# Performance work log

Hardware: AMD Instinct MI355X
Metric: run time of the kernel (lower is better)

The kernel has to match this reference:

```python
import jax, jax.numpy as jnp
import numpy as np
jax.config.update("jax_enable_x64", True)

SR = 44100
STATE_SIZE = 4096
RG0, R10, C10, C20 = 1.0e6, 4.7e5, 3.3e-9, 1.0e-9

# Reconstructed DK-method incidence matrices (3 circuit nodes, 1 vsrc):
#   Vin at node1; C1 node1->node2; R1 node2->gnd; pot top node2->node3;
#   pot bottom node3->gnd; C2 node3->gnd; output at node3 (pot wiper).
_Nu = np.array([[1., 0., 0.]])
_Nx = np.array([[1., -1., 0.], [0., 0., 1.]])
_Nr = np.array([[0., 1., 0.]])
_Nv = np.array([[0., 1., -1.], [0., 0., 1.]])
_No = np.array([[0., 0., 1.]])


def _preamp_forward(x, cond, state, alpha_rg, alpha_r1, alpha_c1, alpha_c2, cond_w, cond_b):
    f64 = jnp.float64
    T = 1.0 / SR
    Nu, Nx, Nr, Nv, No = (jnp.asarray(m, f64) for m in (_Nu, _Nx, _Nr, _Nv, _No))
    Zm = jnp.eye(2, dtype=f64)
    n_nodes, n_vsrc = 3, 1
    zpad = jnp.zeros((2, n_vsrc), f64)
    Nvp = jnp.concatenate([Nv, zpad], axis=1)                      # [2,4]
    Nxp = jnp.concatenate([Nx, zpad], axis=1)                      # [2,4]
    Nop = jnp.concatenate([No, jnp.zeros((1, n_vsrc), f64)], 1)    # [1,4]
    Nup = jnp.concatenate([jnp.zeros((n_nodes, n_vsrc), f64), jnp.eye(n_vsrc, dtype=f64)], 0)  # [4,1]

    # component updates (sigmoid-trimmed around nominal values)
    RG = (0.9 + jax.nn.sigmoid(alpha_rg[0]).astype(f64) * 0.2) * RG0
    R1 = (0.99 + jax.nn.sigmoid(alpha_r1[0]).astype(f64) * 0.02) * R10
    C1 = (0.9 + jax.nn.sigmoid(alpha_c1[0]).astype(f64) * 0.2) * C10
    C2 = (0.9 + jax.nn.sigmoid(alpha_c2[0]).astype(f64) * 0.2) * C20
    Gr = jnp.reshape(1.0 / R1, (1, 1))
    Gx = jnp.diag(jnp.stack([2.0 * C1 / T, 2.0 * C2 / T]))

    # cond block: affine -> sigmoid -> log pot taper
    pot = jax.nn.sigmoid(cond[:, 0] * cond_w[0] + cond_b[0])
    p = jnp.clip((jnp.power(10.0, pot) - 1.0) / 9.0, 1e-4, 1.0 - 1e-4).astype(f64)  # [B]

    # state-space update
    top = jnp.concatenate([Nr.T @ Gr @ Nr + Nx.T @ Gx @ Nx, Nu.T], axis=1)
    bot = jnp.concatenate([Nu, jnp.zeros((n_vsrc, n_vsrc), f64)], axis=1)
    So_inv = jnp.linalg.inv(jnp.concatenate([top, bot], axis=0))   # [4,4]
    Q = Nvp @ So_inv @ Nvp.T                                        # [2,2]
    Ux = Nxp @ So_inv @ Nvp.T                                       # [2,2]
    Uo = Nop @ So_inv @ Nvp.T                                       # [1,2]
    Uu = Nup.T @ So_inv @ Nvp.T                                     # [1,2]
    ZGx = 2.0 * Zm @ Gx
    Ao = ZGx @ Nxp @ So_inv @ Nxp.T - Zm
    Bo = ZGx @ Nxp @ So_inv @ Nup
    Do = Nop @ So_inv @ Nxp.T
    Eo = Nop @ So_inv @ Nup

    d = jnp.stack([(1.0 - p) * RG, p * RG], axis=-1)                # [B,2]
    Rv = d[:, :, None] * jnp.eye(2, dtype=f64)                      # [B,2,2] diag
    RvQ = jnp.linalg.inv(Rv + Q)                                    # [B,2,2]

    ZGxUx = ZGx @ Ux
    A = Ao - ZGxUx @ RvQ @ Ux.T                                     # [B,2,2]
    Bm = Bo - ZGxUx @ RvQ @ Uu.T                                    # [B,2,1]
    Dm = Do - Uo @ RvQ @ Ux.T                                       # [B,1,2]
    Em = Eo - Uo @ RvQ @ Uu.T                                       # [B,1,1]

    # quadratic characteristic poly [1, -tr, det] (= real part of prod(z-eig))
    def poly2(M):
        tr = M[..., 0, 0] + M[..., 1, 1]
        det = M[..., 0, 0] * M[..., 1, 1] - M[..., 0, 1] * M[..., 1, 0]
        return jnp.stack([jnp.ones_like(tr), -tr, det], axis=-1)    # [B,3]

    den = poly2(A)
    num = poly2(A - Bm @ Dm) + (Em[:, 0] - 1.0) * den

    nb = 1 + STATE_SIZE // 2
    z = jnp.exp(-1j * jnp.linspace(0.0, jnp.pi, nb))                # complex128 [nb]

    def polyval(c):  # Horner, highest degree first
        c = c.astype(jnp.complex128)
        return (c[:, 0, None] * z + c[:, 1, None]) * z + c[:, 2, None]  # [B,nb]

    h = polyval(num) / polyval(den)                                 # [B,nb]

    L = x.shape[1]
    st = jnp.concatenate([state[:, L:, :], x], axis=1).astype(f64)  # [B,S,1]
    sf = jnp.fft.rfft(st, axis=1)                                   # [B,nb,1]
    out = jnp.fft.irfft(sf * h[:, :, None], axis=1).astype(jnp.float32)
    return out[:, -L:, :]


def setup_inputs() -> dict:
    key = jax.random.key(0)
    k0, k1, k2 = jax.random.split(key, 3)
    B, L = 2048, 2048
    return {
        "x": jax.random.normal(k0, (B, L, 1), dtype=jnp.float32),
        "cond": jax.random.uniform(k1, (B, 1), dtype=jnp.float32),
        "state": jax.random.normal(k2, (B, STATE_SIZE, 1), dtype=jnp.float32) * 0.1,
        "alpha_rg": jnp.zeros((1,), jnp.float32),
        "alpha_r1": jnp.zeros((1,), jnp.float32),
        "alpha_c1": jnp.zeros((1,), jnp.float32),
        "alpha_c2": jnp.zeros((1,), jnp.float32),
        "cond_w": jnp.ones((1,), jnp.float32),
        "cond_b": jnp.zeros((1,), jnp.float32),
    }


def reference(x, cond, state, alpha_rg, alpha_r1, alpha_c1, alpha_c2, cond_w, cond_b):
    return _preamp_forward(x, cond, state, alpha_rg, alpha_r1, alpha_c1, alpha_c2, cond_w, cond_b)
```

## Files before the change

### kernel.cpp

```cpp
#include <hip/hip_runtime.h>
#include <math.h>

#define NFFT 4096
#define HALF 2048
#define LSEG 2048
#define SSZ 4096

static __device__ __forceinline__ double sigm_f32(float v) {
    return (double)(1.0f / (1.0f + expf(-v)));
}

static __device__ void inv4(const double a[4][4], double out[4][4]) {
    double m[4][8];
    for (int i = 0; i < 4; ++i) {
        for (int j = 0; j < 4; ++j) { m[i][j] = a[i][j]; m[i][j + 4] = (i == j) ? 1.0 : 0.0; }
    }
    for (int c = 0; c < 4; ++c) {
        int piv = c; double best = fabs(m[c][c]);
        for (int r = c + 1; r < 4; ++r) { double v = fabs(m[r][c]); if (v > best) { best = v; piv = r; } }
        if (piv != c) for (int j = 0; j < 8; ++j) { double t = m[c][j]; m[c][j] = m[piv][j]; m[piv][j] = t; }
        double d = 1.0 / m[c][c];
        for (int j = 0; j < 8; ++j) m[c][j] *= d;
        for (int r = 0; r < 4; ++r) {
            if (r == c) continue;
            double f = m[r][c];
            for (int j = 0; j < 8; ++j) m[r][j] -= f * m[c][j];
        }
    }
    for (int i = 0; i < 4; ++i) for (int j = 0; j < 4; ++j) out[i][j] = m[i][j + 4];
}

__global__ void preamp_coef_kernel(const float* __restrict__ cond,
                                   const float* __restrict__ a_rg,
                                   const float* __restrict__ a_r1,
                                   const float* __restrict__ a_c1,
                                   const float* __restrict__ a_c2,
                                   const float* __restrict__ cond_w,
                                   const float* __restrict__ cond_b,
                                   double* __restrict__ coef, int B) {
    int b = blockIdx.x * blockDim.x + threadIdx.x;
    if (b >= B) return;

    const double T = 1.0 / 44100.0;
    const double RG = (0.9 + sigm_f32(a_rg[0]) * 0.2) * 1.0e6;
    const double R1 = (0.99 + sigm_f32(a_r1[0]) * 0.02) * 4.7e5;
    const double C1 = (0.9 + sigm_f32(a_c1[0]) * 0.2) * 3.3e-9;
    const double C2 = (0.9 + sigm_f32(a_c2[0]) * 0.2) * 1.0e-9;
    const double g1 = 1.0 / R1;
    const double gc1 = 2.0 * C1 / T;
    const double gc2 = 2.0 * C2 / T;

    float zf = cond[b] * cond_w[0] + cond_b[0];
    float pot = 1.0f / (1.0f + expf(-zf));
    float pr = (powf(10.0f, pot) - 1.0f) / 9.0f;
    pr = fminf(fmaxf(pr, 1e-4f), 1.0f - 1e-4f);
    double p = (double)pr;

    double So[4][4] = {
        { gc1,     -gc1,      0.0, 1.0},
        {-gc1,      gc1 + g1, 0.0, 0.0},
        { 0.0,      0.0,      gc2, 0.0},
        { 1.0,      0.0,      0.0, 0.0}};
    double S[4][4];
    inv4(So, S);

    double Q00 = S[1][1] - S[1][2] - S[2][1] + S[2][2];
    double Q01 = S[1][2] - S[2][2];
    double Q10 = S[2][1] - S[2][2];
    double Q11 = S[2][2];

    double Ux00 = S[0][1] - S[0][2] - S[1][1] + S[1][2];
    double Ux01 = S[0][2] - S[1][2];
    double Ux10 = S[2][1] - S[2][2];
    double Ux11 = S[2][2];

    double Uo0 = S[2][1] - S[2][2], Uo1 = S[2][2];
    double Uu0 = S[3][1] - S[3][2], Uu1 = S[3][2];

    double P00 = S[0][0] - S[0][1] - S[1][0] + S[1][1];
    double P01 = S[0][2] - S[1][2];
    double P10 = S[2][0] - S[2][1];
    double P11 = S[2][2];

    double Ao00 = 2.0 * gc1 * P00 - 1.0, Ao01 = 2.0 * gc1 * P01;
    double Ao10 = 2.0 * gc2 * P10,       Ao11 = 2.0 * gc2 * P11 - 1.0;

    double Bo0 = 2.0 * gc1 * (S[0][3] - S[1][3]);
    double Bo1 = 2.0 * gc2 * S[2][3];

    double Do0 = S[2][0] - S[2][1], Do1 = S[2][2];
    double Eo  = S[2][3];

    double T00 = 2.0 * gc1 * Ux00, T01 = 2.0 * gc1 * Ux01;
    double T10 = 2.0 * gc2 * Ux10, T11 = 2.0 * gc2 * Ux11;

    double d0 = (1.0 - p) * RG, d1v = p * RG;
    double M00 = d0 + Q00, M01 = Q01, M10 = Q10, M11 = d1v + Q11;
    double idet = 1.0 / (M00 * M11 - M01 * M10);
    double G00 =  M11 * idet, G01 = -M01 * idet;
    double G10 = -M10 * idet, G11 =  M00 * idet;

    double TG00 = T00 * G00 + T01 * G10, TG01 = T00 * G01 + T01 * G11;
    double TG10 = T10 * G00 + T11 * G10, TG11 = T10 * G01 + T11 * G11;

    double A00 = Ao00 - (TG00 * Ux00 + TG01 * Ux01);
    double A01 = Ao01 - (TG00 * Ux10 + TG01 * Ux11);
    double A10 = Ao10 - (TG10 * Ux00 + TG11 * Ux01);
    double A11 = Ao11 - (TG10 * Ux10 + TG11 * Ux11);

    double Bm0 = Bo0 - (TG00 * Uu0 + TG01 * Uu1);
    double Bm1 = Bo1 - (TG10 * Uu0 + TG11 * Uu1);

    double w0v = Uo0 * G00 + Uo1 * G10, w1v = Uo0 * G01 + Uo1 * G11;
    double Dm0 = Do0 - (w0v * Ux00 + w1v * Ux01);
    double Dm1 = Do1 - (w0v * Ux10 + w1v * Ux11);
    double Em  = Eo  - (w0v * Uu0 + w1v * Uu1);

    double den1 = -(A00 + A11);
    double den2 = A00 * A11 - A01 * A10;
    double Mm00 = A00 - Bm0 * Dm0, Mm01 = A01 - Bm0 * Dm1;
    double Mm10 = A10 - Bm1 * Dm0, Mm11 = A11 - Bm1 * Dm1;
    double num0 = Em;
    double num1 = -(Mm00 + Mm11) + (Em - 1.0) * den1;
    double num2 = (Mm00 * Mm11 - Mm01 * Mm10) + (Em - 1.0) * den2;

    coef[(size_t)b * 5 + 0] = num0;
    coef[(size_t)b * 5 + 1] = num1;
    coef[(size_t)b * 5 + 2] = num2;
    coef[(size_t)b * 5 + 3] = den1;
    coef[(size_t)b * 5 + 4] = den2;
}


static __device__ __forceinline__ float2 cmul(float2 a, float2 b) {
    return make_float2(a.x * b.x - a.y * b.y, a.x * b.y + a.y * b.x);
}
static __device__ __forceinline__ float2 cadd(float2 a, float2 b) { return make_float2(a.x + b.x, a.y + b.y); }
static __device__ __forceinline__ float2 csub(float2 a, float2 b) { return make_float2(a.x - b.x, a.y - b.y); }

static __device__ __forceinline__ int PAD(int i) { return i + (i >> 4); }

template <int SGN>
static __device__ __forceinline__ void dft16(float2 r[16]) {
    const float S = (float)SGN;
    float2 t[16];
#pragma unroll
    for (int n1 = 0; n1 < 4; ++n1) {
        float2 a = r[n1], b = r[n1 + 4], c = r[n1 + 8], d = r[n1 + 12];
        float2 A = cadd(a, c), B = cadd(b, d), C = csub(a, c), D = csub(b, d);
        float2 iD = make_float2(-S * D.y, S * D.x);
        t[n1 * 4 + 0] = cadd(A, B);
        t[n1 * 4 + 1] = cadd(C, iD);
        t[n1 * 4 + 2] = csub(A, B);
        t[n1 * 4 + 3] = csub(C, iD);
    }
    const float CC[10] = {1.f, 0.92387953251f, 0.70710678119f, 0.38268343236f, 0.f,
                          -0.38268343236f, -0.70710678119f, -0.92387953251f, -1.f, -0.92387953251f};
    const float SS[10] = {0.f, 0.38268343236f, 0.70710678119f, 0.92387953251f, 1.f,
                          0.92387953251f, 0.70710678119f, 0.38268343236f, 0.f, -0.38268343236f};
#pragma unroll
    for (int n1 = 1; n1 < 4; ++n1) {
#pragma unroll
        for (int m2 = 1; m2 < 4; ++m2) {
            const int k = n1 * m2;
            t[n1 * 4 + m2] = cmul(t[n1 * 4 + m2], make_float2(CC[k], S * SS[k]));
        }
    }
#pragma unroll
    for (int m2 = 0; m2 < 4; ++m2) {
        float2 a = t[m2], b = t[4 + m2], c = t[8 + m2], d = t[12 + m2];
        float2 A = cadd(a, c), B = cadd(b, d), C = csub(a, c), D = csub(b, d);
        float2 iD = make_float2(-S * D.y, S * D.x);
        r[m2]      = cadd(A, B);
        r[m2 + 4]  = cadd(C, iD);
        r[m2 + 8]  = csub(A, B);
        r[m2 + 12] = csub(C, iD);
    }
}

static __device__ __forceinline__ void twiddle_chain(float2 r[16], float2 w1) {
    float2 w2 = cmul(w1, w1);
    float2 w3 = cmul(w2, w1);
    float2 w4 = cmul(w2, w2);
    float2 w5 = cmul(w4, w1);
    float2 w6 = cmul(w4, w2);
    float2 w7 = cmul(w4, w3);
    float2 w8 = cmul(w4, w4);
    r[1] = cmul(r[1], w1);   r[2] = cmul(r[2], w2);
    r[3] = cmul(r[3], w3);   r[4] = cmul(r[4], w4);
    r[5] = cmul(r[5], w5);   r[6] = cmul(r[6], w6);
    r[7] = cmul(r[7], w7);   r[8] = cmul(r[8], w8);
    r[9]  = cmul(r[9],  cmul(w8, w1));
    r[10] = cmul(r[10], cmul(w8, w2));
    r[11] = cmul(r[11], cmul(w8, w3));
    r[12] = cmul(r[12], cmul(w8, w4));
    r[13] = cmul(r[13], cmul(w8, w5));
    r[14] = cmul(r[14], cmul(w8, w6));
    r[15] = cmul(r[15], cmul(w8, w7));
}

static __device__ __forceinline__ float2 eval_h(double n0, double n1, double n2,
                                                double d1, double d2,
                                                double zr, double zi) {
    double ar = n0 * zr + n1, ai = n0 * zi;
    double nr = ar * zr - ai * zi + n2, ni = ar * zi + ai * zr;
    double br = zr + d1, bi = zi;
    double dr = br * zr - bi * zi + d2, di = br * zi + bi * zr;
    float fnr = (float)nr, fni = (float)ni, fdr = (float)dr, fdi = (float)di;
    float idn = __builtin_amdgcn_rcpf(fdr * fdr + fdi * fdi);
    return make_float2((fnr * fdr + fni * fdi) * idn,
                       (fni * fdr - fnr * fdi) * idn);
}

__global__ __launch_bounds__(256)
void preamp_fft_kernel(const float* __restrict__ x,
                       const float* __restrict__ state,
                       const double* __restrict__ coef,
                       float* __restrict__ out, int B) {
    __shared__ float2 a_s[NFFT + NFFT / 16];

    const int t = threadIdx.x;
    const int b0 = 2 * blockIdx.x;
    const int b1 = (b0 + 1 < B) ? b0 + 1 : b0;

    const float* st0 = state + (size_t)b0 * SSZ + (SSZ - LSEG);
    const float* xb0 = x + (size_t)b0 * LSEG;
    const float* st1 = state + (size_t)b1 * SSZ + (SSZ - LSEG);
    const float* xb1 = x + (size_t)b1 * LSEG;

    for (int i = t; i < NFFT; i += 256) {
        float fa, fb;
        if (i < LSEG) { fa = st0[i]; fb = st1[i]; }
        else          { fa = xb0[i - LSEG]; fb = xb1[i - LSEG]; }
        a_s[PAD(i)] = make_float2(fa, fb);
    }
    __syncthreads();

    const float TW4096 = 0.00153398078788564f;
    const float TW256  = 0.02454369260617026f;

    float2 r[16];

#pragma unroll
    for (int m = 0; m < 16; ++m) r[m] = a_s[PAD(t + 256 * m)];
    dft16<-1>(r);
    {
        float sw, cw;
        __sincosf((float)t * TW4096, &sw, &cw);
        twiddle_chain(r, make_float2(cw, -sw));
    }
#pragma unroll
    for (int m = 0; m < 16; ++m) a_s[PAD(t + 256 * m)] = r[m];
    __syncthreads();

    {
        const int sub = t >> 4, j = t & 15;
        const int base = sub * 256 + j;
#pragma unroll
        for (int m = 0; m < 16; ++m) r[m] = a_s[PAD(base + 16 * m)];
        dft16<-1>(r);
        float sw, cw;
        __sincosf((float)j * TW256, &sw, &cw);
        twiddle_chain(r, make_float2(cw, -sw));
#pragma unroll
        for (int m = 0; m < 16; ++m) a_s[PAD(base + 16 * m)] = r[m];
    }
    __syncthreads();

    {
        const int base = 16 * t;
#pragma unroll
        for (int m = 0; m < 16; ++m) r[m] = a_s[PAD(base + m)];
        dft16<-1>(r);
        const int klo = ((t & 15) << 4) | (t >> 4);
        __syncthreads();
#pragma unroll
        for (int m = 0; m < 16; ++m) a_s[PAD((m << 8) | klo)] = r[m];
    }
    __syncthreads();

    {
        const double na0 = coef[(size_t)b0 * 5 + 0];
        const double na1 = coef[(size_t)b0 * 5 + 1];
        const double na2 = coef[(size_t)b0 * 5 + 2];
        const double da1 = coef[(size_t)b0 * 5 + 3];
        const double da2 = coef[(size_t)b0 * 5 + 4];
        const double nb0 = coef[(size_t)b1 * 5 + 0];
        const double nb1 = coef[(size_t)b1 * 5 + 1];
        const double nb2 = coef[(size_t)b1 * 5 + 2];
        const double db1 = coef[(size_t)b1 * 5 + 3];
        const double db2 = coef[(size_t)b1 * 5 + 4];

        for (int i = t; i <= HALF; i += 256) {
            const int k  = i;
            const int kr = (NFFT - i) & (NFFT - 1);
            float2 Wk = a_s[PAD(k)];
            float2 Wr = a_s[PAD(kr)];
            float Xar = 0.5f * (Wk.x + Wr.x), Xai = 0.5f * (Wk.y - Wr.y);
            float Xbr = 0.5f * (Wk.y + Wr.y), Xbi = 0.5f * (Wr.x - Wk.x);
            float sw, cw;
            __sincosf((float)k * TW4096, &sw, &cw);
            const double zr = (double)cw, zi = -(double)sw;
            float2 Ha = eval_h(na0, na1, na2, da1, da2, zr, zi);
            float2 Hb = eval_h(nb0, nb1, nb2, db1, db2, zr, zi);
            float Yar = Ha.x * Xar - Ha.y * Xai, Yai = Ha.x * Xai + Ha.y * Xar;
            float Ybr = Hb.x * Xbr - Hb.y * Xbi, Ybi = Hb.x * Xbi + Hb.y * Xbr;
            a_s[PAD(k)] = make_float2(Yar - Ybi, Yai + Ybr);
            if (kr != k) a_s[PAD(kr)] = make_float2(Yar + Ybi, Ybr - Yai);
        }
    }
    __syncthreads();

    {
        const int base = 16 * t;
        const int klo = ((t & 15) << 4) | (t >> 4);
#pragma unroll
        for (int m = 0; m < 16; ++m) r[m] = a_s[PAD((m << 8) | klo)];
        dft16<1>(r);
        __syncthreads();
#pragma unroll
        for (int m = 0; m < 16; ++m) a_s[PAD(base + m)] = r[m];
    }
    __syncthreads();

    {
        const int sub = t >> 4, j = t & 15;
        const int base = sub * 256 + j;
#pragma unroll
        for (int m = 0; m < 16; ++m) r[m] = a_s[PAD(base + 16 * m)];
        float sw, cw;
        __sincosf((float)j * TW256, &sw, &cw);
        twiddle_chain(r, make_float2(cw, sw));
        dft16<1>(r);
#pragma unroll
        for (int m = 0; m < 16; ++m) a_s[PAD(base + 16 * m)] = r[m];
    }
    __syncthreads();

    {
#pragma unroll
        for (int m = 0; m < 16; ++m) r[m] = a_s[PAD(t + 256 * m)];
        float sw, cw;
        __sincosf((float)t * TW4096, &sw, &cw);
        twiddle_chain(r, make_float2(cw, sw));
        dft16<1>(r);
        const float scale = 1.0f / (float)NFFT;
        float* ob0 = out + (size_t)b0 * LSEG;
        float* ob1 = out + (size_t)b1 * LSEG;
#pragma unroll
        for (int m = 8; m < 16; ++m) {
            ob0[t + 256 * (m - 8)] = r[m].x * scale;
            if (b1 != b0) ob1[t + 256 * (m - 8)] = r[m].y * scale;
        }
    }
}

extern "C" void kernel_launch(void* const* d_in, const int* in_sizes, int n_in,
                              void* d_out, int out_size, void* d_ws, size_t ws_size,
                              hipStream_t stream) {
    const float* x     = (const float*)d_in[0];
    const float* cond  = (const float*)d_in[1];
    const float* state = (const float*)d_in[2];
    const float* a_rg  = (const float*)d_in[3];
    const float* a_r1  = (const float*)d_in[4];
    const float* a_c1  = (const float*)d_in[5];
    const float* a_c2  = (const float*)d_in[6];
    const float* c_w   = (const float*)d_in[7];
    const float* c_b   = (const float*)d_in[8];
    float* out = (float*)d_out;

    const int B = in_sizes[1];
    double* coef = (double*)d_ws;

    preamp_coef_kernel<<<dim3((B + 255) / 256), dim3(256), 0, stream>>>(
        cond, a_rg, a_r1, a_c1, a_c2, c_w, c_b, coef, B);
    preamp_fft_kernel<<<dim3((B + 1) / 2), dim3(256), 0, stream>>>(x, state, coef, out, B);
}
```

Baseline: 126.2 us.

## Fuse coefficient computation into FFT kernel and evaluate transfer function in fp32

Removes the separate coefficient kernel: two threads per block compute the per-batch filter coefficients (using a closed-form inverse of the 4x4 system instead of Gauss-Jordan) and publish them through shared memory. The frequency-response evaluation is rewritten around u = z-1 using a half-angle sine/cosine and fully float arithmetic, replacing the double-precision polynomial evaluation. This cuts a kernel launch, the global coefficient round-trip and the fp64 work in the spectral multiply, at the risk of reduced accuracy in the filter response near DC.

```diff
diff --git a/kernel.cpp b/kernel.cpp
--- a/kernel.cpp
+++ b/kernel.cpp
@@ -5,131 +5,6 @@
 #define HALF 2048
 #define LSEG 2048
 #define SSZ 4096
-
-static __device__ __forceinline__ double sigm_f32(float v) {
-    return (double)(1.0f / (1.0f + expf(-v)));
-}
-
-static __device__ void inv4(const double a[4][4], double out[4][4]) {
-    double m[4][8];
-    for (int i = 0; i < 4; ++i) {
-        for (int j = 0; j < 4; ++j) { m[i][j] = a[i][j]; m[i][j + 4] = (i == j) ? 1.0 : 0.0; }
-    }
-    for (int c = 0; c < 4; ++c) {
-        int piv = c; double best = fabs(m[c][c]);
-        for (int r = c + 1; r < 4; ++r) { double v = fabs(m[r][c]); if (v > best) { best = v; piv = r; } }
-        if (piv != c) for (int j = 0; j < 8; ++j) { double t = m[c][j]; m[c][j] = m[piv][j]; m[piv][j] = t; }
-        double d = 1.0 / m[c][c];
-        for (int j = 0; j < 8; ++j) m[c][j] *= d;
-        for (int r = 0; r < 4; ++r) {
-            if (r == c) continue;
-            double f = m[r][c];
-            for (int j = 0; j < 8; ++j) m[r][j] -= f * m[c][j];
-        }
-    }
-    for (int i = 0; i < 4; ++i) for (int j = 0; j < 4; ++j) out[i][j] = m[i][j + 4];
-}
-
-__global__ void preamp_coef_kernel(const float* __restrict__ cond,
-                                   const float* __restrict__ a_rg,
-                                   const float* __restrict__ a_r1,
-                                   const float* __restrict__ a_c1,
-                                   const float* __restrict__ a_c2,
-                                   const float* __restrict__ cond_w,
-                                   const float* __restrict__ cond_b,
-                                   double* __restrict__ coef, int B) {
-    int b = blockIdx.x * blockDim.x + threadIdx.x;
-    if (b >= B) return;
-
-    const double T = 1.0 / 44100.0;
-    const double RG = (0.9 + sigm_f32(a_rg[0]) * 0.2) * 1.0e6;
-    const double R1 = (0.99 + sigm_f32(a_r1[0]) * 0.02) * 4.7e5;
-    const double C1 = (0.9 + sigm_f32(a_c1[0]) * 0.2) * 3.3e-9;
-    const double C2 = (0.9 + sigm_f32(a_c2[0]) * 0.2) * 1.0e-9;
-    const double g1 = 1.0 / R1;
-    const double gc1 = 2.0 * C1 / T;
-    const double gc2 = 2.0 * C2 / T;
-
-    float zf = cond[b] * cond_w[0] + cond_b[0];
-    float pot = 1.0f / (1.0f + expf(-zf));
-    float pr = (powf(10.0f, pot) - 1.0f) / 9.0f;
-    pr = fminf(fmaxf(pr, 1e-4f), 1.0f - 1e-4f);
-    double p = (double)pr;
-
-    double So[4][4] = {
-        { gc1,     -gc1,      0.0, 1.0},
-        {-gc1,      gc1 + g1, 0.0, 0.0},
-        { 0.0,      0.0,      gc2, 0.0},
-        { 1.0,      0.0,      0.0, 0.0}};
-    double S[4][4];
-    inv4(So, S);
-
-    double Q00 = S[1][1] - S[1][2] - S[2][1] + S[2][2];
-    double Q01 = S[1][2] - S[2][2];
-    double Q10 = S[2][1] - S[2][2];
-    double Q11 = S[2][2];
-
-    double Ux00 = S[0][1] - S[0][2] - S[1][1] + S[1][2];
-    double Ux01 = S[0][2] - S[1][2];
-    double Ux10 = S[2][1] - S[2][2];
-    double Ux11 = S[2][2];
-
-    double Uo0 = S[2][1] - S[2][2], Uo1 = S[2][2];
-    double Uu0 = S[3][1] - S[3][2], Uu1 = S[3][2];
-
-    double P00 = S[0][0] - S[0][1] - S[1][0] + S[1][1];
-    double P01 = S[0][2] - S[1][2];
-    double P10 = S[2][0] - S[2][1];
-    double P11 = S[2][2];
-
-    double Ao00 = 2.0 * gc1 * P00 - 1.0, Ao01 = 2.0 * gc1 * P01;
-    double Ao10 = 2.0 * gc2 * P10,       Ao11 = 2.0 * gc2 * P11 - 1.0;
-
-    double Bo0 = 2.0 * gc1 * (S[0][3] - S[1][3]);
-    double Bo1 = 2.0 * gc2 * S[2][3];
-
-    double Do0 = S[2][0] - S[2][1], Do1 = S[2][2];
-    double Eo  = S[2][3];
-
-    double T00 = 2.0 * gc1 * Ux00, T01 = 2.0 * gc1 * Ux01;
-    double T10 = 2.0 * gc2 * Ux10, T11 = 2.0 * gc2 * Ux11;
-
-    double d0 = (1.0 - p) * RG, d1v = p * RG;
-    double M00 = d0 + Q00, M01 = Q01, M10 = Q10, M11 = d1v + Q11;
-    double idet = 1.0 / (M00 * M11 - M01 * M10);
-    double G00 =  M11 * idet, G01 = -M01 * idet;
-    double G10 = -M10 * idet, G11 =  M00 * idet;
-
-    double TG00 = T00 * G00 + T01 * G10, TG01 = T00 * G01 + T01 * G11;
-    double TG10 = T10 * G00 + T11 * G10, TG11 = T10 * G01 + T11 * G11;
-
-    double A00 = Ao00 - (TG00 * Ux00 + TG01 * Ux01);
-    double A01 = Ao01 - (TG00 * Ux10 + TG01 * Ux11);
-    double A10 = Ao10 - (TG10 * Ux00 + TG11 * Ux01);
-    double A11 = Ao11 - (TG10 * Ux10 + TG11 * Ux11);
-
-    double Bm0 = Bo0 - (TG00 * Uu0 + TG01 * Uu1);
-    double Bm1 = Bo1 - (TG10 * Uu0 + TG11 * Uu1);
-
-    double w0v = Uo0 * G00 + Uo1 * G10, w1v = Uo0 * G01 + Uo1 * G11;
-    double Dm0 = Do0 - (w0v * Ux00 + w1v * Ux01);
-    double Dm1 = Do1 - (w0v * Ux10 + w1v * Ux11);
-    double Em  = Eo  - (w0v * Uu0 + w1v * Uu1);
-
-    double den1 = -(A00 + A11);
-    double den2 = A00 * A11 - A01 * A10;
-    double Mm00 = A00 - Bm0 * Dm0, Mm01 = A01 - Bm0 * Dm1;
-    double Mm10 = A10 - Bm1 * Dm0, Mm11 = A11 - Bm1 * Dm1;
-    double num0 = Em;
-    double num1 = -(Mm00 + Mm11) + (Em - 1.0) * den1;
-    double num2 = (Mm00 * Mm11 - Mm01 * Mm10) + (Em - 1.0) * den2;
-
-    coef[(size_t)b * 5 + 0] = num0;
-    coef[(size_t)b * 5 + 1] = num1;
-    coef[(size_t)b * 5 + 2] = num2;
-    coef[(size_t)b * 5 + 3] = den1;
-    coef[(size_t)b * 5 + 4] = den2;
-}
 
 
 static __device__ __forceinline__ float2 cmul(float2 a, float2 b) {
@@ -199,25 +74,19 @@
     r[15] = cmul(r[15], cmul(w8, w7));
 }
 
-static __device__ __forceinline__ float2 eval_h(double n0, double n1, double n2,
-                                                double d1, double d2,
-                                                double zr, double zi) {
-    double ar = n0 * zr + n1, ai = n0 * zi;
-    double nr = ar * zr - ai * zi + n2, ni = ar * zi + ai * zr;
-    double br = zr + d1, bi = zi;
-    double dr = br * zr - bi * zi + d2, di = br * zi + bi * zr;
-    float fnr = (float)nr, fni = (float)ni, fdr = (float)dr, fdi = (float)di;
-    float idn = __builtin_amdgcn_rcpf(fdr * fdr + fdi * fdi);
-    return make_float2((fnr * fdr + fni * fdi) * idn,
-                       (fni * fdr - fnr * fdi) * idn);
-}
-
 __global__ __launch_bounds__(256)
 void preamp_fft_kernel(const float* __restrict__ x,
                        const float* __restrict__ state,
-                       const double* __restrict__ coef,
+                       const float* __restrict__ cond,
+                       const float* __restrict__ a_rg,
+                       const float* __restrict__ a_r1,
+                       const float* __restrict__ a_c1,
+                       const float* __restrict__ a_c2,
+                       const float* __restrict__ cond_w,
+                       const float* __restrict__ cond_b,
                        float* __restrict__ out, int B) {
     __shared__ float2 a_s[NFFT + NFFT / 16];
+    __shared__ float cf[10];
 
     const int t = threadIdx.x;
     const int b0 = 2 * blockIdx.x;
@@ -234,10 +103,104 @@
         else          { fa = xb0[i - LSEG]; fb = xb1[i - LSEG]; }
         a_s[PAD(i)] = make_float2(fa, fb);
     }
+
+    if ((t & 127) == 0) {
+        const int who = t >> 7;
+        const int bb = who ? b1 : b0;
+
+        const double T = 1.0 / 44100.0;
+        const double RG = (0.9 + (double)(1.0f / (1.0f + expf(-a_rg[0]))) * 0.2) * 1.0e6;
+        const double R1 = (0.99 + (double)(1.0f / (1.0f + expf(-a_r1[0]))) * 0.02) * 4.7e5;
+        const double C1 = (0.9 + (double)(1.0f / (1.0f + expf(-a_c1[0]))) * 0.2) * 3.3e-9;
+        const double C2 = (0.9 + (double)(1.0f / (1.0f + expf(-a_c2[0]))) * 0.2) * 1.0e-9;
+        const double g1 = 1.0 / R1;
+        const double gc1 = 2.0 * C1 * 44100.0;  (void)T;
+        const double gc2 = 2.0 * C2 * 44100.0;
+
+        float zf = cond[bb] * cond_w[0] + cond_b[0];
+        float pot = 1.0f / (1.0f + expf(-zf));
+        float prf = (powf(10.0f, pot) - 1.0f) / 9.0f;
+        prf = fminf(fmaxf(prf, 1e-4f), 1.0f - 1e-4f);
+        const double p = (double)prf;
+
+        const double ds = gc1 + g1;
+        double S[4][4] = {
+            {0.0, 0.0,        0.0,       1.0},
+            {0.0, 1.0 / ds,   0.0,       gc1 / ds},
+            {0.0, 0.0,        1.0 / gc2, 0.0},
+            {1.0, gc1 / ds,   0.0,       -gc1 * g1 / ds}};
+
+        double Q00 = S[1][1] - S[1][2] - S[2][1] + S[2][2];
+        double Q01 = S[1][2] - S[2][2];
+        double Q10 = S[2][1] - S[2][2];
+        double Q11 = S[2][2];
+
+        double Ux00 = S[0][1] - S[0][2] - S[1][1] + S[1][2];
+        double Ux01 = S[0][2] - S[1][2];
+        double Ux10 = S[2][1] - S[2][2];
+        double Ux11 = S[2][2];
+
+        double Uo0 = S[2][1] - S[2][2], Uo1 = S[2][2];
+        double Uu0 = S[3][1] - S[3][2], Uu1 = S[3][2];
+
+        double P00 = S[0][0] - S[0][1] - S[1][0] + S[1][1];
+        double P01 = S[0][2] - S[1][2];
+        double P10 = S[2][0] - S[2][1];
+        double P11 = S[2][2];
+
+        double Ao00 = 2.0 * gc1 * P00 - 1.0, Ao01 = 2.0 * gc1 * P01;
+        double Ao10 = 2.0 * gc2 * P10,       Ao11 = 2.0 * gc2 * P11 - 1.0;
+
+        double Bo0 = 2.0 * gc1 * (S[0][3] - S[1][3]);
+        double Bo1 = 2.0 * gc2 * S[2][3];
+
+        double Do0 = S[2][0] - S[2][1], Do1 = S[2][2];
+        double Eo  = S[2][3];
+
+        double T00 = 2.0 * gc1 * Ux00, T01 = 2.0 * gc1 * Ux01;
+        double T10 = 2.0 * gc2 * Ux10, T11 = 2.0 * gc2 * Ux11;
+
+        double d0 = (1.0 - p) * RG, d1v = p * RG;
+        double M00 = d0 + Q00, M01 = Q01, M10 = Q10, M11 = d1v + Q11;
+        double idet = 1.0 / (M00 * M11 - M01 * M10);
+        double G00 =  M11 * idet, G01 = -M01 * idet;
+        double G10 = -M10 * idet, G11 =  M00 * idet;
+
+        double TG00 = T00 * G00 + T01 * G10, TG01 = T00 * G01 + T01 * G11;
+        double TG10 = T10 * G00 + T11 * G10, TG11 = T10 * G01 + T11 * G11;
+
+        double A00 = Ao00 - (TG00 * Ux00 + TG01 * Ux01);
+        double A01 = Ao01 - (TG00 * Ux10 + TG01 * Ux11);
+        double A10 = Ao10 - (TG10 * Ux00 + TG11 * Ux01);
+        double A11 = Ao11 - (TG10 * Ux10 + TG11 * Ux11);
+
+        double Bm0 = Bo0 - (TG00 * Uu0 + TG01 * Uu1);
+        double Bm1 = Bo1 - (TG10 * Uu0 + TG11 * Uu1);
+
+        double w0v = Uo0 * G00 + Uo1 * G10, w1v = Uo0 * G01 + Uo1 * G11;
+        double Dm0 = Do0 - (w0v * Ux00 + w1v * Ux01);
+        double Dm1 = Do1 - (w0v * Ux10 + w1v * Ux11);
+        double Em  = Eo  - (w0v * Uu0 + w1v * Uu1);
+
+        double den1 = -(A00 + A11);
+        double den2 = A00 * A11 - A01 * A10;
+        double Mm00 = A00 - Bm0 * Dm0, Mm01 = A01 - Bm0 * Dm1;
+        double Mm10 = A10 - Bm1 * Dm0, Mm11 = A11 - Bm1 * Dm1;
+        double num0 = Em;
+        double num1 = -(Mm00 + Mm11) + (Em - 1.0) * den1;
+        double num2 = (Mm00 * Mm11 - Mm01 * Mm10) + (Em - 1.0) * den2;
+
+        cf[who * 5 + 0] = (float)num0;
+        cf[who * 5 + 1] = (float)num1;
+        cf[who * 5 + 2] = (float)(num0 + num1 + num2);
+        cf[who * 5 + 3] = (float)den1;
+        cf[who * 5 + 4] = (float)(1.0 + den1 + den2);
+    }
     __syncthreads();
 
     const float TW4096 = 0.00153398078788564f;
     const float TW256  = 0.02454369260617026f;
+    const float HW4096 = 0.00076699039394282f;
 
     float2 r[16];
 
@@ -280,16 +243,8 @@
     __syncthreads();
 
     {
-        const double na0 = coef[(size_t)b0 * 5 + 0];
-        const double na1 = coef[(size_t)b0 * 5 + 1];
-        const double na2 = coef[(size_t)b0 * 5 + 2];
-        const double da1 = coef[(size_t)b0 * 5 + 3];
-        const double da2 = coef[(size_t)b0 * 5 + 4];
-        const double nb0 = coef[(size_t)b1 * 5 + 0];
-        const double nb1 = coef[(size_t)b1 * 5 + 1];
-        const double nb2 = coef[(size_t)b1 * 5 + 2];
-        const double db1 = coef[(size_t)b1 * 5 + 3];
-        const double db2 = coef[(size_t)b1 * 5 + 4];
+        const float an0 = cf[0], an1 = cf[1], asn = cf[2], ad1 = cf[3], asd = cf[4];
+        const float bn0 = cf[5], bn1 = cf[6], bsn = cf[7], bd1 = cf[8], bsd = cf[9];
 
         for (int i = t; i <= HALF; i += 256) {
             const int k  = i;
@@ -298,13 +253,26 @@
             float2 Wr = a_s[PAD(kr)];
             float Xar = 0.5f * (Wk.x + Wr.x), Xai = 0.5f * (Wk.y - Wr.y);
             float Xbr = 0.5f * (Wk.y + Wr.y), Xbi = 0.5f * (Wr.x - Wk.x);
-            float sw, cw;
-            __sincosf((float)k * TW4096, &sw, &cw);
-            const double zr = (double)cw, zi = -(double)sw;
-            float2 Ha = eval_h(na0, na1, na2, da1, da2, zr, zi);
-            float2 Hb = eval_h(nb0, nb1, nb2, db1, db2, zr, zi);
-            float Yar = Ha.x * Xar - Ha.y * Xai, Yai = Ha.x * Xai + Ha.y * Xar;
-            float Ybr = Hb.x * Xbr - Hb.y * Xbi, Ybi = Hb.x * Xbi + Hb.y * Xbr;
+            float sh, ch;
+            __sincosf((float)k * HW4096, &sh, &ch);
+            float m2s = -2.0f * sh;
+            float ur = m2s * sh, ui = m2s * ch;
+            float pr = ur + 2.0f;
+            float tar = an0 * pr + an1, tai = an0 * ui;
+            float nr = asn + ur * tar - ui * tai, ni = ur * tai + ui * tar;
+            float tbr = pr + ad1;
+            float dr = asd + ur * tbr - ui * ui, di = ur * ui + ui * tbr;
+            float inv = __builtin_amdgcn_rcpf(dr * dr + di * di);
+            float Har = (nr * dr + ni * di) * inv, Hai = (ni * dr - nr * di) * inv;
+            tar = bn0 * pr + bn1; tai = bn0 * ui;
+            nr = bsn + ur * tar - ui * tai; ni = ur * tai + ui * tar;
+            tbr = pr + bd1;
+            dr = bsd + ur * tbr - ui * ui; di = ur * ui + ui * tbr;
+            inv = __builtin_amdgcn_rcpf(dr * dr + di * di);
+            float Hbr = (nr * dr + ni * di) * inv, Hbi = (ni * dr - nr * di) * inv;
+
+            float Yar = Har * Xar - Hai * Xai, Yai = Har * Xai + Hai * Xar;
+            float Ybr = Hbr * Xbr - Hbi * Xbi, Ybi = Hbr * Xbi + Hbi * Xbr;
             a_s[PAD(k)] = make_float2(Yar - Ybi, Yai + Ybr);
             if (kr != k) a_s[PAD(kr)] = make_float2(Yar + Ybi, Ybr - Yai);
         }
@@ -370,9 +338,7 @@
     float* out = (float*)d_out;
 
     const int B = in_sizes[1];
-    double* coef = (double*)d_ws;
-
-    preamp_coef_kernel<<<dim3((B + 255) / 256), dim3(256), 0, stream>>>(
-        cond, a_rg, a_r1, a_c1, a_c2, c_w, c_b, coef, B);
-    preamp_fft_kernel<<<dim3((B + 1) / 2), dim3(256), 0, stream>>>(x, state, coef, out, B);
-}
+
+    preamp_fft_kernel<<<dim3((B + 1) / 2), dim3(256), 0, stream>>>(
+        x, state, cond, a_rg, a_r1, a_c1, a_c2, c_w, c_b, out, B);
+}
```

After: 121.4 us. -3.8%, faster.
